# Kernel tuning notes

Hardware: AMD Instinct MI355X
Metric: run time of the kernel (lower is better)

The kernel has to match this reference:

```python
import jax, jax.numpy as jnp
import numpy as np

B, OUT, EXC_IN, INH_IN, BF = 8192, 1024, 4096, 2048, 4
K_EXC, K_INH = 32, 16


def _pruned_weight(pre_w, K):
    # TopKLinear.pruned_weight: mask of top-K entries (by pre_w) times exp(pre_w)
    w = jnp.exp(pre_w)                      # param_space='log'
    _, idx = jax.lax.top_k(pre_w, K)        # [out, K] indices per row
    rows = jnp.arange(pre_w.shape[0])[:, None]
    mask = jnp.zeros_like(pre_w).at[rows, idx].set(1.0)
    return mask * w


def setup_inputs() -> dict:
    key = jax.random.key(0)
    ks = jax.random.split(key, 5)
    return {
        "x": jax.random.normal(ks[0], (B, EXC_IN), jnp.float32),
        "inhibitory_input": jax.random.normal(ks[1], (B, INH_IN), jnp.float32),
        "branch_input": jax.random.normal(ks[2], (B, OUT * BF), jnp.float32),
        "pre_w_exc": jax.random.uniform(ks[3], (OUT, EXC_IN), jnp.float32, -2.1, -2.0),
        "pre_w_inh": jax.random.uniform(ks[4], (OUT, INH_IN), jnp.float32, -2.1, -2.0),
        "w_block": jnp.ones((OUT, BF), jnp.float32),          # BlockLinear weight (init ones, frozen)
        "presigmoid_Vth": jnp.full((OUT,), -2.0, jnp.float32),  # uniform(-2,-2) == constant
        "log_alpha_max": jnp.zeros((OUT,), jnp.float32),
    }


def reference(x, inhibitory_input, branch_input, pre_w_exc, pre_w_inh,
              w_block, presigmoid_Vth, log_alpha_max):
    # TopKLinear forward: x @ pruned_weight.T
    excitation = x @ _pruned_weight(pre_w_exc, K_EXC).T            # [B, OUT]
    inhibition = inhibitory_input @ _pruned_weight(pre_w_inh, K_INH).T  # [B, OUT]

    # BlockLinear: scatter w_block into block-diagonal [OUT, OUT*BF] then mm;
    # equivalent contraction over the block dim only.
    current = jnp.einsum('nob,ob->no', branch_input.reshape(B, OUT, BF), w_block)
    conductance = jnp.sum(w_block, axis=1)                         # [OUT]

    numerator = excitation + current
    denominator = excitation + 1.0 + conductance + inhibition
    voltage = numerator / denominator

    # reactivation
    Vth = jax.nn.sigmoid(presigmoid_Vth)
    V_diff = voltage - Vth
    rate = jnp.exp(log_alpha_max) * V_diff * V_diff
    return jnp.where(V_diff < 0, jnp.zeros((), voltage.dtype), rate)
```

## Files before the change

kernel.cpp:

```cpp
#include <hip/hip_runtime.h>
#include <cstdint>
#include <cstddef>

#define B_ROWS 8192
#define OUT_N  1024
#define EXC_IN 4096
#define INH_IN 2048
#define K_EXC  32
#define K_INH  16
#define TILE_N 4

template<int COLS, int K>
__global__ __launch_bounds__(256) void topk_kernel(const float* __restrict__ pre_w,
                                                   float2* __restrict__ out_w)
{
    const int row  = blockIdx.x;
    const int tid  = threadIdx.x;
    const int lane = tid & 63;
    const int wave = tid >> 6;
    constexpr int ELEMS = COLS / 256;

    __shared__ unsigned long long red[5];

    const float* src = pre_w + (size_t)row * COLS;
    unsigned long long keys[ELEMS];
#pragma unroll
    for (int i = 0; i < ELEMS; ++i) {
        const int idx = tid + i * 256;
        unsigned int u = __float_as_uint(src[idx]);
        unsigned int m = (u >> 31) ? ~u : (u | 0x80000000u);
        keys[i] = ((unsigned long long)m << 12) | (unsigned long long)(4095 - idx);
    }

#pragma unroll 1
    for (int r = 0; r < K; ++r) {
        unsigned long long best = 0ull;
#pragma unroll
        for (int i = 0; i < ELEMS; ++i) best = (keys[i] > best) ? keys[i] : best;
#pragma unroll
        for (int m = 32; m > 0; m >>= 1) {
            unsigned long long o = __shfl_xor(best, m, 64);
            best = (o > best) ? o : best;
        }
        if (lane == 0) red[wave] = best;
        __syncthreads();
        if (tid == 0) {
            unsigned long long b = red[0];
            b = (red[1] > b) ? red[1] : b;
            b = (red[2] > b) ? red[2] : b;
            b = (red[3] > b) ? red[3] : b;
            red[4] = b;
        }
        __syncthreads();
        const unsigned long long win = red[4];

        if (tid == 0) {
            const unsigned int idx = 4095u - (unsigned int)(win & 0xFFFull);
            const unsigned int m   = (unsigned int)(win >> 12);
            const unsigned int u   = (m >> 31) ? (m & 0x7FFFFFFFu) : ~m;
            const float v = __uint_as_float(u);
            out_w[(size_t)row * K + r] = make_float2(expf(v), __uint_as_float(idx));
        }
#pragma unroll
        for (int i = 0; i < ELEMS; ++i) keys[i] = (keys[i] == win) ? 0ull : keys[i];
    }
}

__global__ __launch_bounds__(256, 2) void dendritic_main_kernel(
    const float*  __restrict__ x,
    const float*  __restrict__ inh,
    const float4* __restrict__ branch,
    const float2* __restrict__ wexc,
    const float2* __restrict__ winh,
    const float4* __restrict__ wblock,
    const float*  __restrict__ presig,
    const float*  __restrict__ logalpha,
    float*        __restrict__ out)
{
    __shared__ float sx[TILE_N * EXC_IN];

    const int tid = threadIdx.x;
    const int n0  = blockIdx.x * TILE_N;

    {
        const float4* xs  = (const float4*)(x + (size_t)n0 * EXC_IN);
        float4*       sx4 = (float4*)sx;
#pragma unroll
        for (int i = 0; i < (TILE_N * EXC_IN / 4) / 256; ++i)
            sx4[tid + i * 256] = xs[tid + i * 256];
    }
    __syncthreads();

    float acc_e[4][TILE_N];
#pragma unroll
    for (int j = 0; j < 4; ++j)
#pragma unroll
        for (int n = 0; n < TILE_N; ++n) acc_e[j][n] = 0.f;

#pragma unroll
    for (int j = 0; j < 4; ++j) {
        const int o = tid + j * 256;
        const float2* wr = wexc + (size_t)o * K_EXC;
#pragma unroll 4
        for (int k = 0; k < K_EXC; ++k) {
            const float2 wv = wr[k];
            const int c = (int)__float_as_uint(wv.y);
            const float* p = sx + c;
#pragma unroll
            for (int n = 0; n < TILE_N; ++n)
                acc_e[j][n] = fmaf(p[n * EXC_IN], wv.x, acc_e[j][n]);
        }
    }
    __syncthreads();

    {
        const float4* is4 = (const float4*)(inh + (size_t)n0 * INH_IN);
        float4*       sx4 = (float4*)sx;
#pragma unroll
        for (int i = 0; i < (TILE_N * INH_IN / 4) / 256; ++i)
            sx4[tid + i * 256] = is4[tid + i * 256];
    }
    __syncthreads();

    float acc_i[4][TILE_N];
#pragma unroll
    for (int j = 0; j < 4; ++j)
#pragma unroll
        for (int n = 0; n < TILE_N; ++n) acc_i[j][n] = 0.f;

#pragma unroll
    for (int j = 0; j < 4; ++j) {
        const int o = tid + j * 256;
        const float2* wr = winh + (size_t)o * K_INH;
#pragma unroll 4
        for (int k = 0; k < K_INH; ++k) {
            const float2 wv = wr[k];
            const int c = (int)__float_as_uint(wv.y);
            const float* p = sx + c;
#pragma unroll
            for (int n = 0; n < TILE_N; ++n)
                acc_i[j][n] = fmaf(p[n * INH_IN], wv.x, acc_i[j][n]);
        }
    }

#pragma unroll
    for (int j = 0; j < 4; ++j) {
        const int o = tid + j * 256;
        const float4 wb = wblock[o];
        const float cond  = wb.x + wb.y + wb.z + wb.w;
        const float Vth   = 1.f / (1.f + expf(-presig[o]));
        const float alpha = expf(logalpha[o]);
#pragma unroll
        for (int n = 0; n < TILE_N; ++n) {
            const float4 br = branch[(size_t)(n0 + n) * 1024 + o];
            const float cur = br.x * wb.x + br.y * wb.y + br.z * wb.z + br.w * wb.w;
            const float e  = acc_e[j][n];
            const float ii = acc_i[j][n];
            const float num = e + cur;
            const float den = e + 1.f + cond + ii;
            const float v   = num / den;
            const float d   = v - Vth;
            const float r   = alpha * d * d;
            out[(size_t)(n0 + n) * OUT_N + o] = (d < 0.f) ? 0.f : r;
        }
    }
}

extern "C" void kernel_launch(void* const* d_in, const int* in_sizes, int n_in,
                              void* d_out, int out_size, void* d_ws, size_t ws_size,
                              hipStream_t stream)
{
    const float* x      = (const float*)d_in[0];
    const float* inh    = (const float*)d_in[1];
    const float* branch = (const float*)d_in[2];
    const float* pwe    = (const float*)d_in[3];
    const float* pwi    = (const float*)d_in[4];
    const float* wb     = (const float*)d_in[5];
    const float* ps     = (const float*)d_in[6];
    const float* la     = (const float*)d_in[7];
    float* out = (float*)d_out;

    float2* wexc = (float2*)d_ws;
    float2* winh = (float2*)((char*)d_ws + (size_t)OUT_N * K_EXC * sizeof(float2));

    topk_kernel<EXC_IN, K_EXC><<<OUT_N, 256, 0, stream>>>(pwe, wexc);
    topk_kernel<INH_IN, K_INH><<<OUT_N, 256, 0, stream>>>(pwi, winh);

    dendritic_main_kernel<<<B_ROWS / TILE_N, 256, 0, stream>>>(
        x, inh, (const float4*)branch, wexc, winh,
        (const float4*)wb, ps, la, out);
}
```

Baseline: 464.5 us.

## Use wave-per-row top-k and interleave activation tiles in shared memory

The two block-per-row top-k kernels become one launch where each 64-lane wave selects top-K for one row, using only wave shuffles, so the per-round __syncthreads and shared-memory reductions go away. In the main kernel, activations are transposed in registers via shuffles while staged, so the four batch rows for each column sit in one float4. The sparse gather then does a single 128-bit LDS per index instead of four scalar loads. The cost is more serial work per wave in top-k, with each lane holding up to 64 keys in registers, plus extra shuffle instructions during staging.

```diff
diff --git a/kernel.cpp b/kernel.cpp
--- a/kernel.cpp
+++ b/kernel.cpp
@@ -11,59 +11,76 @@
 #define TILE_N 4
 
 template<int COLS, int K>
-__global__ __launch_bounds__(256) void topk_kernel(const float* __restrict__ pre_w,
-                                                   float2* __restrict__ out_w)
-{
-    const int row  = blockIdx.x;
-    const int tid  = threadIdx.x;
-    const int lane = tid & 63;
-    const int wave = tid >> 6;
-    constexpr int ELEMS = COLS / 256;
-
-    __shared__ unsigned long long red[5];
-
-    const float* src = pre_w + (size_t)row * COLS;
-    unsigned long long keys[ELEMS];
-#pragma unroll
-    for (int i = 0; i < ELEMS; ++i) {
-        const int idx = tid + i * 256;
-        unsigned int u = __float_as_uint(src[idx]);
-        unsigned int m = (u >> 31) ? ~u : (u | 0x80000000u);
-        keys[i] = ((unsigned long long)m << 12) | (unsigned long long)(4095 - idx);
-    }
-
+__device__ __forceinline__ void topk_row(const float* __restrict__ src,
+                                         float2* __restrict__ orow, int lane)
+{
+    constexpr int E4 = COLS / 256;
+    unsigned long long keys[E4 * 4];
+#pragma unroll
+    for (int i = 0; i < E4; ++i) {
+        const float4 v = ((const float4*)src)[i * 64 + lane];
+        const float vv[4] = {v.x, v.y, v.z, v.w};
+#pragma unroll
+        for (int q = 0; q < 4; ++q) {
+            const int idx = (i * 64 + lane) * 4 + q;
+            const unsigned int u = __float_as_uint(vv[q]);
+            const unsigned int m = (u >> 31) ? ~u : (u | 0x80000000u);
+            keys[i * 4 + q] = ((unsigned long long)m << 12)
+                            | (unsigned long long)(4095 - idx);
+        }
+    }
+
+    unsigned long long win = 0xFFFFFFFFFFFFFFFFull;
 #pragma unroll 1
     for (int r = 0; r < K; ++r) {
         unsigned long long best = 0ull;
 #pragma unroll
-        for (int i = 0; i < ELEMS; ++i) best = (keys[i] > best) ? keys[i] : best;
-#pragma unroll
-        for (int m = 32; m > 0; m >>= 1) {
-            unsigned long long o = __shfl_xor(best, m, 64);
+        for (int i = 0; i < E4 * 4; ++i) {
+            const unsigned long long k2 = (keys[i] == win) ? 0ull : keys[i];
+            keys[i] = k2;
+            best = (k2 > best) ? k2 : best;
+        }
+#pragma unroll
+        for (int m = 1; m < 64; m <<= 1) {
+            const unsigned long long o = __shfl_xor(best, m, 64);
             best = (o > best) ? o : best;
         }
-        if (lane == 0) red[wave] = best;
-        __syncthreads();
-        if (tid == 0) {
-            unsigned long long b = red[0];
-            b = (red[1] > b) ? red[1] : b;
-            b = (red[2] > b) ? red[2] : b;
-            b = (red[3] > b) ? red[3] : b;
-            red[4] = b;
-        }
-        __syncthreads();
-        const unsigned long long win = red[4];
-
-        if (tid == 0) {
+        win = best;
+        if (lane == 0) {
             const unsigned int idx = 4095u - (unsigned int)(win & 0xFFFull);
-            const unsigned int m   = (unsigned int)(win >> 12);
-            const unsigned int u   = (m >> 31) ? (m & 0x7FFFFFFFu) : ~m;
+            const unsigned int mm  = (unsigned int)(win >> 12);
+            const unsigned int u   = (mm & 0x80000000u) ? (mm & 0x7FFFFFFFu) : ~mm;
             const float v = __uint_as_float(u);
-            out_w[(size_t)row * K + r] = make_float2(expf(v), __uint_as_float(idx));
-        }
-#pragma unroll
-        for (int i = 0; i < ELEMS; ++i) keys[i] = (keys[i] == win) ? 0ull : keys[i];
-    }
+            orow[r] = make_float2(expf(v), __uint_as_float(idx));
+        }
+    }
+}
+
+__global__ __launch_bounds__(256, 1) void topk_both_kernel(
+    const float* __restrict__ pwe, const float* __restrict__ pwi,
+    float2* __restrict__ wexc, float2* __restrict__ winh)
+{
+    const int wid  = (blockIdx.x * 256 + threadIdx.x) >> 6;
+    const int lane = threadIdx.x & 63;
+    if (wid < OUT_N) {
+        topk_row<EXC_IN, K_EXC>(pwe + (size_t)wid * EXC_IN,
+                                wexc + (size_t)wid * K_EXC, lane);
+    } else {
+        const int r = wid - OUT_N;
+        topk_row<INH_IN, K_INH>(pwi + (size_t)r * INH_IN,
+                                winh + (size_t)r * K_INH, lane);
+    }
+}
+
+__device__ __forceinline__ float4 xpose4(float4 v, int j)
+{
+    const float u0 = __shfl_xor(v.y, 1, 64), u1 = __shfl_xor(v.x, 1, 64);
+    const float u2 = __shfl_xor(v.w, 1, 64), u3 = __shfl_xor(v.z, 1, 64);
+    if (j & 1) { v.x = u0; v.z = u2; } else { v.y = u1; v.w = u3; }
+    const float w0 = __shfl_xor(v.z, 2, 64), w1 = __shfl_xor(v.w, 2, 64);
+    const float w2 = __shfl_xor(v.x, 2, 64), w3 = __shfl_xor(v.y, 2, 64);
+    if (j & 2) { v.x = w0; v.y = w1; } else { v.z = w2; v.w = w3; }
+    return v;
 }
 
 __global__ __launch_bounds__(256, 2) void dendritic_main_kernel(
@@ -77,17 +94,19 @@
     const float*  __restrict__ logalpha,
     float*        __restrict__ out)
 {
-    __shared__ float sx[TILE_N * EXC_IN];
+    __shared__ float sx[EXC_IN * TILE_N];
 
     const int tid = threadIdx.x;
     const int n0  = blockIdx.x * TILE_N;
-
-    {
-        const float4* xs  = (const float4*)(x + (size_t)n0 * EXC_IN);
-        float4*       sx4 = (float4*)sx;
-#pragma unroll
-        for (int i = 0; i < (TILE_N * EXC_IN / 4) / 256; ++i)
-            sx4[tid + i * 256] = xs[tid + i * 256];
+    const int jq  = tid & 3;
+    const int c4b = tid >> 2;
+
+#pragma unroll
+    for (int it = 0; it < (EXC_IN * TILE_N / 4) / 256; ++it) {
+        const int c4 = c4b + it * 64;
+        float4 v = ((const float4*)(x + (size_t)(n0 + jq) * EXC_IN))[c4];
+        v = xpose4(v, jq);
+        ((float4*)sx)[it * 256 + tid] = v;
     }
     __syncthreads();
 
@@ -101,24 +120,25 @@
     for (int j = 0; j < 4; ++j) {
         const int o = tid + j * 256;
         const float2* wr = wexc + (size_t)o * K_EXC;
-#pragma unroll 4
+#pragma unroll 8
         for (int k = 0; k < K_EXC; ++k) {
             const float2 wv = wr[k];
             const int c = (int)__float_as_uint(wv.y);
-            const float* p = sx + c;
-#pragma unroll
-            for (int n = 0; n < TILE_N; ++n)
-                acc_e[j][n] = fmaf(p[n * EXC_IN], wv.x, acc_e[j][n]);
+            const float4 xv = ((const float4*)sx)[c];
+            acc_e[j][0] = fmaf(xv.x, wv.x, acc_e[j][0]);
+            acc_e[j][1] = fmaf(xv.y, wv.x, acc_e[j][1]);
+            acc_e[j][2] = fmaf(xv.z, wv.x, acc_e[j][2]);
+            acc_e[j][3] = fmaf(xv.w, wv.x, acc_e[j][3]);
         }
     }
     __syncthreads();
 
-    {
-        const float4* is4 = (const float4*)(inh + (size_t)n0 * INH_IN);
-        float4*       sx4 = (float4*)sx;
-#pragma unroll
-        for (int i = 0; i < (TILE_N * INH_IN / 4) / 256; ++i)
-            sx4[tid + i * 256] = is4[tid + i * 256];
+#pragma unroll
+    for (int it = 0; it < (INH_IN * TILE_N / 4) / 256; ++it) {
+        const int c4 = c4b + it * 64;
+        float4 v = ((const float4*)(inh + (size_t)(n0 + jq) * INH_IN))[c4];
+        v = xpose4(v, jq);
+        ((float4*)sx)[it * 256 + tid] = v;
     }
     __syncthreads();
 
@@ -132,14 +152,15 @@
     for (int j = 0; j < 4; ++j) {
         const int o = tid + j * 256;
         const float2* wr = winh + (size_t)o * K_INH;
-#pragma unroll 4
+#pragma unroll 8
         for (int k = 0; k < K_INH; ++k) {
             const float2 wv = wr[k];
             const int c = (int)__float_as_uint(wv.y);
-            const float* p = sx + c;
-#pragma unroll
-            for (int n = 0; n < TILE_N; ++n)
-                acc_i[j][n] = fmaf(p[n * INH_IN], wv.x, acc_i[j][n]);
+            const float4 xv = ((const float4*)sx)[c];
+            acc_i[j][0] = fmaf(xv.x, wv.x, acc_i[j][0]);
+            acc_i[j][1] = fmaf(xv.y, wv.x, acc_i[j][1]);
+            acc_i[j][2] = fmaf(xv.z, wv.x, acc_i[j][2]);
+            acc_i[j][3] = fmaf(xv.w, wv.x, acc_i[j][3]);
         }
     }
 
@@ -152,7 +173,7 @@
         const float alpha = expf(logalpha[o]);
 #pragma unroll
         for (int n = 0; n < TILE_N; ++n) {
-            const float4 br = branch[(size_t)(n0 + n) * 1024 + o];
+            const float4 br = branch[(size_t)(n0 + n) * OUT_N + o];
             const float cur = br.x * wb.x + br.y * wb.y + br.z * wb.z + br.w * wb.w;
             const float e  = acc_e[j][n];
             const float ii = acc_i[j][n];
@@ -183,8 +204,7 @@
     float2* wexc = (float2*)d_ws;
     float2* winh = (float2*)((char*)d_ws + (size_t)OUT_N * K_EXC * sizeof(float2));
 
-    topk_kernel<EXC_IN, K_EXC><<<OUT_N, 256, 0, stream>>>(pwe, wexc);
-    topk_kernel<INH_IN, K_INH><<<OUT_N, 256, 0, stream>>>(pwi, winh);
+    topk_both_kernel<<<(2 * OUT_N) / 4, 256, 0, stream>>>(pwe, pwi, wexc, winh);
 
     dendritic_main_kernel<<<B_ROWS / TILE_N, 256, 0, stream>>>(
         x, inh, (const float4*)branch, wexc, winh,
```

Measured after the change: 457.5 us. Within noise of the previous version (-1.5%).
